# Kernel tuning notes

Measured on AMD Instinct MI355X. Metric: run time of the kernel, lower is better.

## Reference

```python
import jax, jax.numpy as jnp
import numpy as np

B, N, L, E = 4096, 64, 256, 256


def setup_inputs() -> dict:
    key = jax.random.key(0)
    k1, k2, k3, k4, k5, k6 = jax.random.split(key, 6)
    return {
        "agent_latent": jax.random.normal(k1, (B, L), dtype=jnp.float32),
        "opponent_latents": jax.random.normal(k2, (B, N, L), dtype=jnp.float32),
        "hard_attention": jax.random.uniform(k3, (B, N), dtype=jnp.float32),
        "Ws": jax.random.normal(k4, (E, L), dtype=jnp.float32) * (2.0 / (L + E)) ** 0.5,
        "Wt": jax.random.normal(k5, (E, L), dtype=jnp.float32) * (2.0 / (L + E)) ** 0.5,
        "Wc": jax.random.normal(k6, (E, L), dtype=jnp.float32) * (2.0 / (L + E)) ** 0.5,
    }


def reference(agent_latent, opponent_latents, hard_attention, Ws, Wt, Wc):
    # agent embedding: [B, E]  (nn.Linear: x @ W.T)
    a = agent_latent @ Ws.T
    # opponent key embedding: [B, N, E]
    emb_t = jnp.einsum('bnl,el->bne', opponent_latents, Wt)
    # bmm([B,N,E],[B,E,1]) -> [B,N]
    scores = jnp.einsum('bne,be->bn', emb_t, a)
    scores = jax.nn.softmax(scores, axis=-1) * hard_attention
    # opponent value embedding: [B, N, E]
    emb_c = jnp.einsum('bnl,el->bne', opponent_latents, Wc)
    # broadcast-multiply + sum over opponents -> [B, E]
    result = jnp.einsum('bn,bne->be', scores, emb_c)
    return result, scores
```

## Files before the change

kernel.cpp:

```cpp
#include <hip/hip_runtime.h>


#define Bsz 4096
#define Nn  64
#define Ll  256
#define Ee  256

__device__ __forceinline__ void gload_lds16(const float4* g, float4* lds_base) {
  __builtin_amdgcn_global_load_lds(
      (const __attribute__((address_space(1))) unsigned int*)g,
      (__attribute__((address_space(3))) unsigned int*)lds_base,
      16, 0, 0);
}

__global__ __launch_bounds__(256) void prep_kernel(
    const float* __restrict__ Ws, const float* __restrict__ Wt,
    const float* __restrict__ Wc, float* __restrict__ MT, float* __restrict__ WcT) {
  int col = threadIdx.x;
  int row = blockIdx.x;
  if (row < 256) {
    float acc = 0.f;
    for (int e = 0; e < 256; ++e)
      acc = fmaf(Ws[e * 256 + row], Wt[e * 256 + col], acc);
    MT[row * 256 + col] = acc;
  } else {
    int l = row - 256;
    WcT[l * 256 + col] = Wc[col * 256 + l];
  }
}

__global__ __launch_bounds__(256, 2) void mega_kernel(
    const float* __restrict__ agent, const float* __restrict__ opp,
    const float* __restrict__ hard, const float* __restrict__ MT,
    const float* __restrict__ WcT, float* __restrict__ out,
    float* __restrict__ scores_out) {
  __shared__ float opp_s[Nn * Ll];
  __shared__ float V_s[8 * Ll];
  __shared__ float sraw[Nn];
  __shared__ float sfin[Nn];

  const int tid = threadIdx.x;
  const int lane = tid & 63;
  const int wave = tid >> 6;
  const int b0 = blockIdx.x * 8;

  const int jq = lane;
  const int r0 = wave * 2;

  float* ag_s  = opp_s;
  float* T_tmp = opp_s + 2048;
  {
    const float4* in4 = (const float4*)(agent + (size_t)b0 * 256);
    float4* s4 = (float4*)ag_s;
    s4[tid] = in4[tid];
    s4[256 + tid] = in4[256 + tid];
    __syncthreads();

    float4 a0 = {0.f, 0.f, 0.f, 0.f};
    float4 a1 = {0.f, 0.f, 0.f, 0.f};
    for (int k4 = 0; k4 < 64; ++k4) {
      const float4 w0 = ((const float4*)(MT + (k4 * 4 + 0) * 256))[jq];
      const float4 w1 = ((const float4*)(MT + (k4 * 4 + 1) * 256))[jq];
      const float4 w2 = ((const float4*)(MT + (k4 * 4 + 2) * 256))[jq];
      const float4 w3 = ((const float4*)(MT + (k4 * 4 + 3) * 256))[jq];
      const float4 v0 = ((const float4*)(ag_s + (r0 + 0) * 256))[k4];
      const float4 v1 = ((const float4*)(ag_s + (r0 + 1) * 256))[k4];
      a0.x = fmaf(v0.x, w0.x, fmaf(v0.y, w1.x, fmaf(v0.z, w2.x, fmaf(v0.w, w3.x, a0.x))));
      a0.y = fmaf(v0.x, w0.y, fmaf(v0.y, w1.y, fmaf(v0.z, w2.y, fmaf(v0.w, w3.y, a0.y))));
      a0.z = fmaf(v0.x, w0.z, fmaf(v0.y, w1.z, fmaf(v0.z, w2.z, fmaf(v0.w, w3.z, a0.z))));
      a0.w = fmaf(v0.x, w0.w, fmaf(v0.y, w1.w, fmaf(v0.z, w2.w, fmaf(v0.w, w3.w, a0.w))));
      a1.x = fmaf(v1.x, w0.x, fmaf(v1.y, w1.x, fmaf(v1.z, w2.x, fmaf(v1.w, w3.x, a1.x))));
      a1.y = fmaf(v1.x, w0.y, fmaf(v1.y, w1.y, fmaf(v1.z, w2.y, fmaf(v1.w, w3.y, a1.y))));
      a1.z = fmaf(v1.x, w0.z, fmaf(v1.y, w1.z, fmaf(v1.z, w2.z, fmaf(v1.w, w3.z, a1.z))));
      a1.w = fmaf(v1.x, w0.w, fmaf(v1.y, w1.w, fmaf(v1.z, w2.w, fmaf(v1.w, w3.w, a1.w))));
    }
    __syncthreads();
    ((float4*)(T_tmp + (r0 + 0) * 256))[jq] = a0;
    ((float4*)(T_tmp + (r0 + 1) * 256))[jq] = a1;
    __syncthreads();
  }
  float4 tv[8];
#pragma unroll
  for (int i = 0; i < 8; ++i) tv[i] = ((const float4*)(T_tmp + i * 256))[lane];
  __syncthreads();

  const float4* o4base = (const float4*)(opp + (size_t)b0 * (Nn * Ll));
  float4* os4 = (float4*)opp_s;
#pragma unroll
  for (int i = 0; i < 8; ++i) {
    const float4* o4 = o4base + (size_t)i * 4096;
#pragma unroll
    for (int k = 0; k < 16; ++k)
      gload_lds16(o4 + k * 256 + wave * 64 + lane, os4 + k * 256 + wave * 64);
    __syncthreads();

    const float4 tvi = tv[i];
    for (int jj = 0; jj < 16; ++jj) {
      const int n = wave * 16 + jj;
      const float4 ov = ((const float4*)(opp_s + n * Ll))[lane];
      float p = ov.x * tvi.x + ov.y * tvi.y + ov.z * tvi.z + ov.w * tvi.w;
#pragma unroll
      for (int off = 32; off; off >>= 1) p += __shfl_down(p, off, 64);
      if (lane == 0) sraw[n] = p;
    }
    __syncthreads();

    if (tid < 64) {
      const float x = sraw[tid];
      float m = x;
#pragma unroll
      for (int off = 32; off; off >>= 1) m = fmaxf(m, __shfl_xor(m, off, 64));
      const float e = __expf(x - m);
      float s = e;
#pragma unroll
      for (int off = 32; off; off >>= 1) s += __shfl_xor(s, off, 64);
      const float val = e / s * hard[(size_t)(b0 + i) * Nn + tid];
      sfin[tid] = val;
      scores_out[(size_t)(b0 + i) * Nn + tid] = val;
    }
    __syncthreads();

    float acc = 0.f;
#pragma unroll
    for (int n = 0; n < Nn; ++n) acc = fmaf(sfin[n], opp_s[n * Ll + tid], acc);
    V_s[i * Ll + tid] = acc;
    __syncthreads();
  }

  {
    float4 a0 = {0.f, 0.f, 0.f, 0.f};
    float4 a1 = {0.f, 0.f, 0.f, 0.f};
    for (int k4 = 0; k4 < 64; ++k4) {
      const float4 w0 = ((const float4*)(WcT + (k4 * 4 + 0) * 256))[jq];
      const float4 w1 = ((const float4*)(WcT + (k4 * 4 + 1) * 256))[jq];
      const float4 w2 = ((const float4*)(WcT + (k4 * 4 + 2) * 256))[jq];
      const float4 w3 = ((const float4*)(WcT + (k4 * 4 + 3) * 256))[jq];
      const float4 v0 = ((const float4*)(V_s + (r0 + 0) * 256))[k4];
      const float4 v1 = ((const float4*)(V_s + (r0 + 1) * 256))[k4];
      a0.x = fmaf(v0.x, w0.x, fmaf(v0.y, w1.x, fmaf(v0.z, w2.x, fmaf(v0.w, w3.x, a0.x))));
      a0.y = fmaf(v0.x, w0.y, fmaf(v0.y, w1.y, fmaf(v0.z, w2.y, fmaf(v0.w, w3.y, a0.y))));
      a0.z = fmaf(v0.x, w0.z, fmaf(v0.y, w1.z, fmaf(v0.z, w2.z, fmaf(v0.w, w3.z, a0.z))));
      a0.w = fmaf(v0.x, w0.w, fmaf(v0.y, w1.w, fmaf(v0.z, w2.w, fmaf(v0.w, w3.w, a0.w))));
      a1.x = fmaf(v1.x, w0.x, fmaf(v1.y, w1.x, fmaf(v1.z, w2.x, fmaf(v1.w, w3.x, a1.x))));
      a1.y = fmaf(v1.x, w0.y, fmaf(v1.y, w1.y, fmaf(v1.z, w2.y, fmaf(v1.w, w3.y, a1.y))));
      a1.z = fmaf(v1.x, w0.z, fmaf(v1.y, w1.z, fmaf(v1.z, w2.z, fmaf(v1.w, w3.z, a1.z))));
      a1.w = fmaf(v1.x, w0.w, fmaf(v1.y, w1.w, fmaf(v1.z, w2.w, fmaf(v1.w, w3.w, a1.w))));
    }
    ((float4*)(out + (size_t)(b0 + r0 + 0) * 256))[jq] = a0;
    ((float4*)(out + (size_t)(b0 + r0 + 1) * 256))[jq] = a1;
  }
}

extern "C" void kernel_launch(void* const* d_in, const int* in_sizes, int n_in,
                              void* d_out, int out_size, void* d_ws, size_t ws_size,
                              hipStream_t stream) {
  const float* agent = (const float*)d_in[0];
  const float* opp   = (const float*)d_in[1];
  const float* hard  = (const float*)d_in[2];
  const float* Ws    = (const float*)d_in[3];
  const float* Wt    = (const float*)d_in[4];
  const float* Wc    = (const float*)d_in[5];

  float* out = (float*)d_out;
  float* scores_out = out + (size_t)Bsz * Ee;

  float* ws  = (float*)d_ws;
  float* MT  = ws;
  float* WcT = MT + 65536;

  prep_kernel<<<512, 256, 0, stream>>>(Ws, Wt, Wc, MT, WcT);
  mega_kernel<<<Bsz / 8, 256, 0, stream>>>(agent, opp, hard, MT, WcT, out, scores_out);
}
```

Before: 420.6 us.

## Double-buffer opponent tiles with async LDS loads and widen blocks to 16 batches

Each block now handles 16 batch rows with 512 threads and double-buffers the 64x256 opponent tile in LDS, issuing the next tile's global-to-LDS loads before computing on the current one. The aim is to hide global memory latency that the old load-then-sync pattern exposed each iteration. Full __syncthreads are replaced with explicit lgkmcnt/vmcnt waits plus s_barrier. LDS use roughly doubles (128KB opp_s plus 16KB V_s), which likely limits occupancy to one block per CU despite launch_bounds asking for 2.

```diff
diff --git a/kernel.cpp b/kernel.cpp
--- a/kernel.cpp
+++ b/kernel.cpp
@@ -5,6 +5,10 @@
 #define Nn  64
 #define Ll  256
 #define Ee  256
+
+#define BPB 16
+#define TPB 512
+#define TILE (Nn * Ll)
 
 __device__ __forceinline__ void gload_lds16(const float4* g, float4* lds_base) {
   __builtin_amdgcn_global_load_lds(
@@ -12,6 +16,17 @@
       (__attribute__((address_space(3))) unsigned int*)lds_base,
       16, 0, 0);
 }
+
+#define LGKM0_BAR() do {                                  \
+  asm volatile("s_waitcnt lgkmcnt(0)" ::: "memory");      \
+  __builtin_amdgcn_s_barrier();                           \
+  __builtin_amdgcn_sched_barrier(0);                      \
+} while (0)
+
+#define WAIT_VM(N) do {                                   \
+  asm volatile("s_waitcnt vmcnt(" #N ")" ::: "memory");   \
+  __builtin_amdgcn_sched_barrier(0);                      \
+} while (0)
 
 __global__ __launch_bounds__(256) void prep_kernel(
     const float* __restrict__ Ws, const float* __restrict__ Wt,
@@ -29,32 +44,42 @@
   }
 }
 
-__global__ __launch_bounds__(256, 2) void mega_kernel(
+__global__ __launch_bounds__(TPB, 2) void mega_kernel(
     const float* __restrict__ agent, const float* __restrict__ opp,
     const float* __restrict__ hard, const float* __restrict__ MT,
     const float* __restrict__ WcT, float* __restrict__ out,
     float* __restrict__ scores_out) {
-  __shared__ float opp_s[Nn * Ll];
-  __shared__ float V_s[8 * Ll];
+  __shared__ float opp_s[2 * TILE];
+  __shared__ float V_s[BPB * Ll];
   __shared__ float sraw[Nn];
   __shared__ float sfin[Nn];
 
   const int tid = threadIdx.x;
   const int lane = tid & 63;
   const int wave = tid >> 6;
-  const int b0 = blockIdx.x * 8;
+  const int b0 = blockIdx.x * BPB;
 
   const int jq = lane;
   const int r0 = wave * 2;
 
-  float* ag_s  = opp_s;
-  float* T_tmp = opp_s + 2048;
+  auto stage = [&](int bi, int buf) {
+    const float4* o4 = (const float4*)(opp + (size_t)(b0 + bi) * TILE);
+    float4* os4 = (float4*)(opp_s + buf * TILE);
+#pragma unroll
+    for (int k = 0; k < 8; ++k)
+      gload_lds16(o4 + k * 512 + wave * 64 + lane, os4 + k * 512 + wave * 64);
+  };
+
+  stage(0, 0);
+
+  float* ag_s  = V_s;
+  float* T_tmp = opp_s + TILE;
   {
     const float4* in4 = (const float4*)(agent + (size_t)b0 * 256);
     float4* s4 = (float4*)ag_s;
     s4[tid] = in4[tid];
-    s4[256 + tid] = in4[256 + tid];
-    __syncthreads();
+    s4[TPB + tid] = in4[TPB + tid];
+    LGKM0_BAR();
 
     float4 a0 = {0.f, 0.f, 0.f, 0.f};
     float4 a1 = {0.f, 0.f, 0.f, 0.f};
@@ -74,36 +99,38 @@
       a1.z = fmaf(v1.x, w0.z, fmaf(v1.y, w1.z, fmaf(v1.z, w2.z, fmaf(v1.w, w3.z, a1.z))));
       a1.w = fmaf(v1.x, w0.w, fmaf(v1.y, w1.w, fmaf(v1.z, w2.w, fmaf(v1.w, w3.w, a1.w))));
     }
-    __syncthreads();
     ((float4*)(T_tmp + (r0 + 0) * 256))[jq] = a0;
     ((float4*)(T_tmp + (r0 + 1) * 256))[jq] = a1;
-    __syncthreads();
-  }
-  float4 tv[8];
-#pragma unroll
-  for (int i = 0; i < 8; ++i) tv[i] = ((const float4*)(T_tmp + i * 256))[lane];
-  __syncthreads();
-
-  const float4* o4base = (const float4*)(opp + (size_t)b0 * (Nn * Ll));
-  float4* os4 = (float4*)opp_s;
-#pragma unroll
-  for (int i = 0; i < 8; ++i) {
-    const float4* o4 = o4base + (size_t)i * 4096;
-#pragma unroll
-    for (int k = 0; k < 16; ++k)
-      gload_lds16(o4 + k * 256 + wave * 64 + lane, os4 + k * 256 + wave * 64);
-    __syncthreads();
+    LGKM0_BAR();
+  }
+  float4 tv[BPB];
+#pragma unroll
+  for (int i = 0; i < BPB; ++i) tv[i] = ((const float4*)(T_tmp + i * 256))[lane];
+  LGKM0_BAR();
+
+#pragma unroll
+  for (int i = 0; i < BPB; ++i) {
+    float* cur = opp_s + (i & 1) * TILE;
+    if (i < BPB - 1) {
+      stage(i + 1, (i + 1) & 1);
+      WAIT_VM(8);
+    } else {
+      WAIT_VM(0);
+    }
+    __builtin_amdgcn_s_barrier();
+    __builtin_amdgcn_sched_barrier(0);
 
     const float4 tvi = tv[i];
-    for (int jj = 0; jj < 16; ++jj) {
-      const int n = wave * 16 + jj;
-      const float4 ov = ((const float4*)(opp_s + n * Ll))[lane];
+#pragma unroll
+    for (int jj = 0; jj < 8; ++jj) {
+      const int n = wave * 8 + jj;
+      const float4 ov = ((const float4*)(cur + n * Ll))[lane];
       float p = ov.x * tvi.x + ov.y * tvi.y + ov.z * tvi.z + ov.w * tvi.w;
 #pragma unroll
       for (int off = 32; off; off >>= 1) p += __shfl_down(p, off, 64);
       if (lane == 0) sraw[n] = p;
     }
-    __syncthreads();
+    LGKM0_BAR();
 
     if (tid < 64) {
       const float x = sraw[tid];
@@ -118,13 +145,15 @@
       sfin[tid] = val;
       scores_out[(size_t)(b0 + i) * Nn + tid] = val;
     }
-    __syncthreads();
-
-    float acc = 0.f;
-#pragma unroll
-    for (int n = 0; n < Nn; ++n) acc = fmaf(sfin[n], opp_s[n * Ll + tid], acc);
-    V_s[i * Ll + tid] = acc;
-    __syncthreads();
+    LGKM0_BAR();
+
+    if (tid < Ll) {
+      float acc = 0.f;
+#pragma unroll
+      for (int n = 0; n < Nn; ++n) acc = fmaf(sfin[n], cur[n * Ll + tid], acc);
+      V_s[i * Ll + tid] = acc;
+    }
+    LGKM0_BAR();
   }
 
   {
@@ -169,5 +198,5 @@
   float* WcT = MT + 65536;
 
   prep_kernel<<<512, 256, 0, stream>>>(Ws, Wt, Wc, MT, WcT);
-  mega_kernel<<<Bsz / 8, 256, 0, stream>>>(agent, opp, hard, MT, WcT, out, scores_out);
-}
+  mega_kernel<<<Bsz / BPB, TPB, 0, stream>>>(agent, opp, hard, MT, WcT, out, scores_out);
+}
```

Result: no change. 424.6 us (+1.0%).
